# Kernel tuning notes

Measured on AMD Instinct MI355X. Metric: run time of the kernel, lower is better.

## Reference

```python
import jax, jax.numpy as jnp
import numpy as np

VOCAB = 50257
C = 8  # n_dim_categories
B, T = 4, 4096


def setup_inputs() -> dict:
    key = jax.random.key(0)
    k1, k2, k3 = jax.random.split(key, 3)
    token_ids = jax.random.randint(k1, (B, T), 0, VOCAB)
    dim_embedding = jax.random.normal(k2, (VOCAB, C), dtype=jnp.float32)
    compatibility = jax.random.normal(k3, (C, C), dtype=jnp.float32) * 0.1
    return {"token_ids": token_ids, "dim_embedding": dim_embedding,
            "compatibility": compatibility}


def reference(token_ids, dim_embedding, compatibility):
    # (B,T,C): embedding lookup then softmax over categories
    dim_probs = jax.nn.softmax(dim_embedding[token_ids], axis=-1)
    # bilinear compatibility over all T x T token pairs -> (B,T,T)
    compat = jnp.einsum('btc,cd,bsd->bts', dim_probs, compatibility, dim_probs)
    mask_bias = jax.nn.sigmoid(compat) * 2 - 1
    return mask_bias
```

## Files before the change

### kernel.cpp

```cpp
#include <hip/hip_runtime.h>
#include <hip/hip_bf16.h>

typedef float f32x4 __attribute__((ext_vector_type(4)));

namespace {
constexpr int kB = 4;
constexpr int kT = 4096;
constexpr int kC = 8;
constexpr int kTRows = 16;
constexpr int kSPerThread = 4;
constexpr int kBlockThreads = 256;
constexpr int kSTile = kBlockThreads * kSPerThread;
}

__device__ __forceinline__ void softmax8(const float e[kC], float p[kC]) {
    float m = e[0];
#pragma unroll
    for (int i = 1; i < kC; ++i) m = fmaxf(m, e[i]);
    float sum = 0.f;
#pragma unroll
    for (int i = 0; i < kC; ++i) { p[i] = __expf(e[i] - m); sum += p[i]; }
    float inv = __builtin_amdgcn_rcpf(sum);
#pragma unroll
    for (int i = 0; i < kC; ++i) p[i] *= inv;
}

__device__ __forceinline__ void load_emb_row(const float* __restrict__ emb, int tok,
                                             float e[kC]) {
    const f32x4* row = reinterpret_cast<const f32x4*>(emb) + (size_t)tok * 2;
    f32x4 e0 = row[0], e1 = row[1];
    e[0] = e0.x; e[1] = e0.y; e[2] = e0.z; e[3] = e0.w;
    e[4] = e1.x; e[5] = e1.y; e[6] = e1.z; e[7] = e1.w;
}

__global__ __launch_bounds__(256) void dam_fused(const int* __restrict__ token_ids,
                                                 const float* __restrict__ emb,
                                                 const float* __restrict__ cmat,
                                                 float* __restrict__ out) {
    const int b = blockIdx.z;
    const int t0 = blockIdx.y * kTRows;
    const int s0 = blockIdx.x * kSTile;
    const int tid = threadIdx.x;

    __shared__ f32x4 p_lds[kTRows * 2];

    if (tid < kTRows) {
        int tok = token_ids[b * kT + t0 + tid];
        float e[kC], p[kC];
        load_emb_row(emb, tok, e);
        softmax8(e, p);
        p_lds[tid * 2 + 0] = f32x4{p[0], p[1], p[2], p[3]};
        p_lds[tid * 2 + 1] = f32x4{p[4], p[5], p[6], p[7]};
    }

    const int s = s0 + tid * kSPerThread;
    int4 toks = *reinterpret_cast<const int4*>(&token_ids[b * kT + s]);
    int tokj[kSPerThread] = {toks.x, toks.y, toks.z, toks.w};
    float z[kSPerThread][kC];
#pragma unroll
    for (int j = 0; j < kSPerThread; ++j) {
        float e[kC], q[kC];
        load_emb_row(emb, tokj[j], e);
        softmax8(e, q);
#pragma unroll
        for (int c = 0; c < kC; ++c) {
            float acc = 0.f;
#pragma unroll
            for (int d = 0; d < kC; ++d) acc = fmaf(cmat[c * kC + d], q[d], acc);
            z[j][c] = -acc;
        }
    }

    __syncthreads();

    float* orow = out + ((size_t)(b * kT + t0)) * kT + s;
#pragma unroll
    for (int tt = 0; tt < kTRows; ++tt) {
        f32x4 p0 = p_lds[tt * 2 + 0];
        f32x4 p1 = p_lds[tt * 2 + 1];
        float pr[kC] = {p0.x, p0.y, p0.z, p0.w, p1.x, p1.y, p1.z, p1.w};
        float r[kSPerThread];
#pragma unroll
        for (int j = 0; j < kSPerThread; ++j) {
            float acc = 0.f;
#pragma unroll
            for (int i = 0; i < kC; ++i) acc = fmaf(pr[i], z[j][i], acc);
            float ex = __expf(acc);
            r[j] = (1.f - ex) * __builtin_amdgcn_rcpf(1.f + ex);
        }
        f32x4 ov = {r[0], r[1], r[2], r[3]};
        *reinterpret_cast<f32x4*>(orow + (size_t)tt * kT) = ov;
    }
}

extern "C" void kernel_launch(void* const* d_in, const int* in_sizes, int n_in,
                              void* d_out, int out_size, void* d_ws, size_t ws_size,
                              hipStream_t stream) {
    const int* token_ids = (const int*)d_in[0];
    const float* emb     = (const float*)d_in[1];
    const float* cmat    = (const float*)d_in[2];
    float* out = (float*)d_out;

    dim3 grid(kT / kSTile, kT / kTRows, kB);
    dam_fused<<<grid, kBlockThreads, 0, stream>>>(token_ids, emb, cmat, out);
}
```

Measured before the change: 56.30 us.

## Enlarge T-row tile and issue all embedding loads up front

```diff
diff --git a/kernel.cpp b/kernel.cpp
--- a/kernel.cpp
+++ b/kernel.cpp
@@ -7,7 +7,7 @@
 constexpr int kB = 4;
 constexpr int kT = 4096;
 constexpr int kC = 8;
-constexpr int kTRows = 16;
+constexpr int kTRows = 64;
 constexpr int kSPerThread = 4;
 constexpr int kBlockThreads = 256;
 constexpr int kSTile = kBlockThreads * kSPerThread;
@@ -25,14 +25,6 @@
     for (int i = 0; i < kC; ++i) p[i] *= inv;
 }
 
-__device__ __forceinline__ void load_emb_row(const float* __restrict__ emb, int tok,
-                                             float e[kC]) {
-    const f32x4* row = reinterpret_cast<const f32x4*>(emb) + (size_t)tok * 2;
-    f32x4 e0 = row[0], e1 = row[1];
-    e[0] = e0.x; e[1] = e0.y; e[2] = e0.z; e[3] = e0.w;
-    e[4] = e1.x; e[5] = e1.y; e[6] = e1.z; e[7] = e1.w;
-}
-
 __global__ __launch_bounds__(256) void dam_fused(const int* __restrict__ token_ids,
                                                  const float* __restrict__ emb,
                                                  const float* __restrict__ cmat,
@@ -44,23 +36,40 @@
 
     __shared__ f32x4 p_lds[kTRows * 2];
 
+    f32x4 pe0, pe1;
     if (tid < kTRows) {
-        int tok = token_ids[b * kT + t0 + tid];
-        float e[kC], p[kC];
-        load_emb_row(emb, tok, e);
+        int tokT = token_ids[b * kT + t0 + tid];
+        const f32x4* prow = reinterpret_cast<const f32x4*>(emb) + (size_t)tokT * 2;
+        pe0 = prow[0];
+        pe1 = prow[1];
+    }
+
+    const int s = s0 + tid * kSPerThread;
+    int4 toks = *reinterpret_cast<const int4*>(&token_ids[b * kT + s]);
+    int tokS[kSPerThread] = {toks.x, toks.y, toks.z, toks.w};
+    f32x4 se[kSPerThread][2];
+#pragma unroll
+    for (int j = 0; j < kSPerThread; ++j) {
+        const f32x4* srow = reinterpret_cast<const f32x4*>(emb) + (size_t)tokS[j] * 2;
+        se[j][0] = srow[0];
+        se[j][1] = srow[1];
+    }
+
+    if (tid < kTRows) {
+        float e[kC] = {pe0.x, pe0.y, pe0.z, pe0.w, pe1.x, pe1.y, pe1.z, pe1.w};
+        float p[kC];
         softmax8(e, p);
         p_lds[tid * 2 + 0] = f32x4{p[0], p[1], p[2], p[3]};
         p_lds[tid * 2 + 1] = f32x4{p[4], p[5], p[6], p[7]};
     }
+    __syncthreads();
 
-    const int s = s0 + tid * kSPerThread;
-    int4 toks = *reinterpret_cast<const int4*>(&token_ids[b * kT + s]);
-    int tokj[kSPerThread] = {toks.x, toks.y, toks.z, toks.w};
     float z[kSPerThread][kC];
 #pragma unroll
     for (int j = 0; j < kSPerThread; ++j) {
-        float e[kC], q[kC];
-        load_emb_row(emb, tokj[j], e);
+        float e[kC] = {se[j][0].x, se[j][0].y, se[j][0].z, se[j][0].w,
+                       se[j][1].x, se[j][1].y, se[j][1].z, se[j][1].w};
+        float q[kC];
         softmax8(e, q);
 #pragma unroll
         for (int c = 0; c < kC; ++c) {
@@ -71,10 +80,8 @@
         }
     }
 
-    __syncthreads();
-
     float* orow = out + ((size_t)(b * kT + t0)) * kT + s;
-#pragma unroll
+#pragma unroll 4
     for (int tt = 0; tt < kTRows; ++tt) {
         f32x4 p0 = p_lds[tt * 2 + 0];
         f32x4 p1 = p_lds[tt * 2 + 1];
```

New measurement: 50.04 us. 1.12x faster.
